# Kernel tuning notes

Measured on AMD Instinct MI355X. Metric: run time of the kernel, lower is better.

## Reference

```python
import jax, jax.numpy as jnp
import numpy as np


def setup_inputs() -> dict:
    key = jax.random.key(0)
    ks = jax.random.split(key, 6)
    B, H, W, C = 4, 64, 64, 256
    D = 256 // 4  # inter_channel // 4
    return {
        "g": jax.random.normal(ks[0], (B, H, W, C), dtype=jnp.float32),
        "x": jax.random.normal(ks[1], (B, H, W, C), dtype=jnp.float32),
        "x_query": jax.random.normal(ks[2], (B, H, W, D), dtype=jnp.float32),
        "phi_g": jax.random.normal(ks[3], (B, H, W, D), dtype=jnp.float32),
        "x_value": jax.random.normal(ks[4], (B, H, W, C), dtype=jnp.float32),
        "k": jax.random.normal(ks[5], (1,), dtype=jnp.float32),
    }


def reference(g, x, x_query, phi_g, x_value, k):
    B, H, W, C = x.shape
    D = x_query.shape[-1]
    HW = H * W
    q = x_query.reshape(B, HW, D)
    pg = phi_g.reshape(B, HW, D)
    v = x_value.reshape(B, HW, C)
    # scale[b,i,j] = sum_d phi_g[b,i,d] * x_query[b,j,d]  -> (B, HW, HW)
    scale = jnp.einsum("bid,bjd->bij", pg, q)
    soft = jax.nn.softmax(scale, axis=-1)
    # scaled_value[b,i,c] = sum_j soft[b,i,j] * v[b,j,c]
    sv = jnp.einsum("bij,bjc->bic", soft, v).reshape(B, H, W, C)
    layero = k * sv + x
    return jnp.concatenate([layero, g], axis=3)
```

## Files before the change

kernel.cpp:

```cpp
#include <hip/hip_runtime.h>

#define N_  4096
#define D_  64
#define C_  256

typedef short bf16x8 __attribute__((ext_vector_type(8)));
typedef float f32x4  __attribute__((ext_vector_type(4)));

__device__ __forceinline__ unsigned short f2bf(float f) {
    union { float f; unsigned int i; } v; v.f = f;
    unsigned int r = v.i + 0x7fffu + ((v.i >> 16) & 1u);
    return (unsigned short)(r >> 16);
}

__global__ void prepass_kernel(const float* __restrict__ xq,
                               const float* __restrict__ pg,
                               const float* __restrict__ xv,
                               unsigned short* __restrict__ qbf,
                               unsigned short* __restrict__ pgbf,
                               unsigned short* __restrict__ vt2) {
    const int bid = blockIdx.x;
    const int t   = threadIdx.x;
    if (bid < 512) {
        const float* src = (bid < 256) ? xq : pg;
        unsigned short* dst = (bid < 256) ? qbf : pgbf;
        const int base = (bid & 255) * 1024 + t;
#pragma unroll
        for (int it = 0; it < 4; ++it) {
            const int i = base + it * 256;
            float4 v = ((const float4*)src)[i];
            ushort4 o;
            o.x = f2bf(v.x); o.y = f2bf(v.y); o.z = f2bf(v.z); o.w = f2bf(v.w);
            ((ushort4*)dst)[i] = o;
        }
        return;
    }
    const int lane = t & 63;
    const int w    = t >> 6;
    const int l15  = lane & 15;
    const int quad = lane >> 4;
    const int f    = (bid - 512) * 4 + w;
    const int b    = f >> 11;
    const int jt   = (f >> 6) & 31;
    const int cb   = (f >> 2) & 15;
    const int ks   = f & 3;
    const int c    = cb * 16 + l15;
    const int jb   = jt * 128 + ks * 32 + quad * 8;
    const float* src = xv + ((size_t)b * N_ + jb) * C_ + c;
    float v0 = src[0 * C_], v1 = src[1 * C_], v2 = src[2 * C_], v3 = src[3 * C_];
    float v4 = src[4 * C_], v5 = src[5 * C_], v6 = src[6 * C_], v7 = src[7 * C_];
    uint4 o;
    o.x = (unsigned)f2bf(v0) | ((unsigned)f2bf(v1) << 16);
    o.y = (unsigned)f2bf(v2) | ((unsigned)f2bf(v3) << 16);
    o.z = (unsigned)f2bf(v4) | ((unsigned)f2bf(v5) << 16);
    o.w = (unsigned)f2bf(v6) | ((unsigned)f2bf(v7) << 16);
    *(uint4*)(vt2 + (size_t)f * 512 + lane * 8) = o;
}

__global__ __launch_bounds__(512, 2) void attn_main(
    const float* __restrict__ g,  const float* __restrict__ x,
    const float* __restrict__ kk, float* __restrict__ out,
    const unsigned short* __restrict__ qbf,
    const unsigned short* __restrict__ pgbf,
    const unsigned short* __restrict__ vt2)
{
    __shared__ __align__(16) unsigned char smem[69632];
    __shared__ float s_l[64];

    const int t    = threadIdx.x;
    const int lane = t & 63;
    const int w    = t >> 6;
    const int l15  = lane & 15;
    const int quad = lane >> 4;
    const int swz  = (l15 & 7) << 4;
    const int jh   = w >> 2;
    const int ch4  = w & 3;

    const int bid = blockIdx.x;
    const int b   = bid & 3;
    const int rg  = bid >> 2;
    const int i0  = rg * 64;
    const size_t rowbase = (size_t)b * N_ + i0;

    if (t < 64) s_l[t] = 0.f;

#pragma unroll
    for (int it = 0; it < 8; ++it) {
        const int row = it * 8 + w;
        const int c4  = lane * 4;
        const float4 gv = *(const float4*)(g + (rowbase + row) * C_ + c4);
        *(float4*)(out + (rowbase + row) * (2 * C_) + C_ + c4) = gv;
    }

    bf16x8 pgf[4][2];
#pragma unroll
    for (int nt = 0; nt < 4; ++nt)
#pragma unroll
        for (int ks = 0; ks < 2; ++ks)
            pgf[nt][ks] = *(const bf16x8*)(pgbf +
                (rowbase + nt * 16 + l15) * D_ + ks * 32 + quad * 8);

    f32x4 oacc[4][4];
#pragma unroll
    for (int mt = 0; mt < 4; ++mt)
#pragma unroll
        for (int ct = 0; ct < 4; ++ct)
            oacc[mt][ct] = (f32x4){0.f, 0.f, 0.f, 0.f};
    float ls[4] = {0.f, 0.f, 0.f, 0.f};

    const unsigned short* qb  = qbf + (size_t)b * N_ * D_;
    const unsigned short* vtb = vt2 + (size_t)b * N_ * C_;
    unsigned short* const pb0 = (unsigned short*)smem;
    unsigned short* const pb1 = (unsigned short*)(smem + 16384);

    auto load_q = [&](bf16x8 (&qf)[2], int jt) {
#pragma unroll
        for (int ks = 0; ks < 2; ++ks)
            qf[ks] = *(const bf16x8*)(qb +
                (size_t)(jt * 128 + w * 16 + l15) * D_ + ks * 32 + quad * 8);
    };
    auto load_v = [&](bf16x8 (&vf)[2][4], int jt) {
#pragma unroll
        for (int ks2 = 0; ks2 < 2; ++ks2)
#pragma unroll
            for (int ct = 0; ct < 4; ++ct)
                vf[ks2][ct] = *(const bf16x8*)(vtb +
                    ((size_t)(jt * 16 + ch4 * 4 + ct) * 4 + (jh * 2 + ks2)) * 512 +
                    (size_t)lane * 8);
    };
    auto s_step = [&](const bf16x8 (&qf)[2], unsigned short* pbuf) {
        f32x4 sacc[4];
#pragma unroll
        for (int nt = 0; nt < 4; ++nt) sacc[nt] = (f32x4){0.f,0.f,0.f,0.f};
#pragma unroll
        for (int ks = 0; ks < 2; ++ks)
#pragma unroll
            for (int nt = 0; nt < 4; ++nt)
                sacc[nt] = __builtin_amdgcn_mfma_f32_16x16x32_bf16(
                    qf[ks], pgf[nt][ks], sacc[nt], 0, 0, 0);
#pragma unroll
        for (int nt = 0; nt < 4; ++nt) {
            const float p0 = __expf(sacc[nt][0]);
            const float p1 = __expf(sacc[nt][1]);
            const float p2 = __expf(sacc[nt][2]);
            const float p3 = __expf(sacc[nt][3]);
            ls[nt] += (p0 + p1) + (p2 + p3);
            ushort4 pk;
            pk.x = f2bf(p0); pk.y = f2bf(p1); pk.z = f2bf(p2); pk.w = f2bf(p3);
            const int wb = ((nt * 16 + l15) * 256 + (w * 16 + quad * 4) * 2) ^ swz;
            *(ushort4*)((char*)pbuf + wb) = pk;
        }
    };
    auto pv_step = [&](const bf16x8 (&vf)[2][4], const unsigned short* pbuf) {
#pragma unroll
        for (int ks2 = 0; ks2 < 2; ++ks2) {
            const int ks = jh * 2 + ks2;
            bf16x8 pa[4];
#pragma unroll
            for (int mt = 0; mt < 4; ++mt) {
                const int rb = ((mt * 16 + l15) * 256 + ks * 64 + quad * 16) ^ swz;
                pa[mt] = *(const bf16x8*)((const char*)pbuf + rb);
            }
#pragma unroll
            for (int ct = 0; ct < 4; ++ct)
#pragma unroll
                for (int mt = 0; mt < 4; ++mt)
                    oacc[mt][ct] = __builtin_amdgcn_mfma_f32_16x16x32_bf16(
                        pa[mt], vf[ks2][ct], oacc[mt][ct], 0, 0, 0);
        }
    };

    bf16x8 qfA[2], qfB[2], vfA[2][4], vfB[2][4];

    load_q(qfA, 0);
    load_v(vfA, 0);
    s_step(qfA, pb0);
    load_q(qfB, 1);
    __syncthreads();

#pragma unroll 1
    for (int jtp = 0; jtp < 15; ++jtp) {
        const int p = 2 * jtp;
        load_v(vfB, p + 1);
        load_q(qfA, p + 2);
        s_step(qfB, pb1);
        pv_step(vfA, pb0);
        __syncthreads();
        load_v(vfA, p + 2);
        load_q(qfB, p + 3);
        s_step(qfA, pb0);
        pv_step(vfB, pb1);
        __syncthreads();
    }
    load_v(vfB, 31);
    s_step(qfB, pb1);
    pv_step(vfA, pb0);
    __syncthreads();
    pv_step(vfB, pb1);

#pragma unroll
    for (int nt = 0; nt < 4; ++nt) {
        float s = ls[nt];
        s += __shfl_xor(s, 16);
        s += __shfl_xor(s, 32);
        if (lane < 16) atomicAdd(&s_l[nt * 16 + lane], s);
    }
    __syncthreads();

    {
        float* Rg = (float*)(smem + (size_t)ch4 * 17408);
        if (jh == 1) {
#pragma unroll
            for (int mt = 0; mt < 4; ++mt)
#pragma unroll
                for (int ct = 0; ct < 4; ++ct)
#pragma unroll
                    for (int r = 0; r < 4; ++r)
                        Rg[(mt * 16 + quad * 4 + r) * 68 + ct * 16 + l15] = oacc[mt][ct][r];
        }
        __syncthreads();
        if (jh == 0) {
#pragma unroll
            for (int mt = 0; mt < 4; ++mt)
#pragma unroll
                for (int ct = 0; ct < 4; ++ct)
#pragma unroll
                    for (int r = 0; r < 4; ++r) {
                        const int idx = (mt * 16 + quad * 4 + r) * 68 + ct * 16 + l15;
                        Rg[idx] += oacc[mt][ct][r];
                    }
        }
        __syncthreads();
    }

    const float kval = kk[0];
#pragma unroll
    for (int it = 0; it < 8; ++it) {
        const int idx = it * 512 + t;
        const int row = idx >> 6;
        const int cq  = idx & 63;
        const int c   = cq * 4;
        const float* Rg = (const float*)(smem + (size_t)(cq >> 4) * 17408);
        const f32x4 ov = *(const f32x4*)&Rg[row * 68 + (cq & 15) * 4];
        const float linv = 1.f / s_l[row];
        const size_t rr = rowbase + row;
        const float4 xv4 = *(const float4*)(x + rr * C_ + c);
        float4 o4;
        o4.x = kval * (ov[0] * linv) + xv4.x;
        o4.y = kval * (ov[1] * linv) + xv4.y;
        o4.z = kval * (ov[2] * linv) + xv4.z;
        o4.w = kval * (ov[3] * linv) + xv4.w;
        *(float4*)(out + rr * (2 * C_) + c) = o4;
    }
}

#define ROWS 4
#define FNT  256
__global__ __launch_bounds__(FNT, 2) void attn_fallback(
    const float* __restrict__ g, const float* __restrict__ x,
    const float* __restrict__ xq, const float* __restrict__ pg,
    const float* __restrict__ xv, const float* __restrict__ kk,
    float* __restrict__ out)
{
    __shared__ __align__(16) float s_pg[ROWS][D_];
    __shared__ __align__(16) float s_sc[N_ * ROWS];
    __shared__ float s_rmax[4][ROWS];
    __shared__ float s_rsum[4][ROWS];

    const int t = threadIdx.x, lane = t & 63, w = t >> 6, blk = blockIdx.x;
    const int b = blk >> 10, i0 = (blk & 1023) * ROWS;
    const size_t rowbase = (size_t)b * N_ + i0;
    {
        const int r = t >> 6, cc = (t & 63) * 4;
        const float4 gv = *(const float4*)(g + (rowbase + r) * C_ + cc);
        *(float4*)(out + (rowbase + r) * (2 * C_) + C_ + cc) = gv;
    }
    { const int r = t >> 6, d = t & 63; s_pg[r][d] = pg[(rowbase + r) * D_ + d]; }
    __syncthreads();
    const float* qb = xq + (size_t)b * N_ * D_;
    float lmax[ROWS];
#pragma unroll
    for (int r = 0; r < ROWS; ++r) lmax[r] = -1e30f;
    for (int jj = 0; jj < N_ / FNT; ++jj) {
        const int j = t + jj * FNT;
        const float4* q4p = (const float4*)(qb + (size_t)j * D_);
        float s[ROWS] = {0.f, 0.f, 0.f, 0.f};
#pragma unroll
        for (int u = 0; u < D_ / 8; ++u) {
            const float4 qa = q4p[u * 2], qc = q4p[u * 2 + 1];
#pragma unroll
            for (int r = 0; r < ROWS; ++r) {
                const float4 pa = *(const float4*)&s_pg[r][u * 8];
                const float4 pb = *(const float4*)&s_pg[r][u * 8 + 4];
                s[r] += qa.x * pa.x + qa.y * pa.y + qa.z * pa.z + qa.w * pa.w
                      + qc.x * pb.x + qc.y * pb.y + qc.z * pb.z + qc.w * pb.w;
            }
        }
        *(float4*)&s_sc[j * ROWS] = make_float4(s[0], s[1], s[2], s[3]);
#pragma unroll
        for (int r = 0; r < ROWS; ++r) lmax[r] = fmaxf(lmax[r], s[r]);
    }
#pragma unroll
    for (int r = 0; r < ROWS; ++r) {
        float m = lmax[r];
        for (int o = 32; o > 0; o >>= 1) m = fmaxf(m, __shfl_down(m, o));
        if (lane == 0) s_rmax[w][r] = m;
    }
    __syncthreads();
    float bmax[ROWS];
#pragma unroll
    for (int r = 0; r < ROWS; ++r)
        bmax[r] = fmaxf(fmaxf(s_rmax[0][r], s_rmax[1][r]), fmaxf(s_rmax[2][r], s_rmax[3][r]));
    float lsum[ROWS] = {0.f, 0.f, 0.f, 0.f};
    for (int jj = 0; jj < N_ / FNT; ++jj) {
        const int j = t + jj * FNT;
        float4 s4 = *(const float4*)&s_sc[j * ROWS];
        s4.x = __expf(s4.x - bmax[0]); s4.y = __expf(s4.y - bmax[1]);
        s4.z = __expf(s4.z - bmax[2]); s4.w = __expf(s4.w - bmax[3]);
        *(float4*)&s_sc[j * ROWS] = s4;
        lsum[0] += s4.x; lsum[1] += s4.y; lsum[2] += s4.z; lsum[3] += s4.w;
    }
#pragma unroll
    for (int r = 0; r < ROWS; ++r) {
        float sm = lsum[r];
        for (int o = 32; o > 0; o >>= 1) sm += __shfl_down(sm, o);
        if (lane == 0) s_rsum[w][r] = sm;
    }
    __syncthreads();
    float rinv[ROWS];
#pragma unroll
    for (int r = 0; r < ROWS; ++r)
        rinv[r] = 1.f / (s_rsum[0][r] + s_rsum[1][r] + s_rsum[2][r] + s_rsum[3][r]);
    const int jg = lane >> 4;
    const int c0 = (w * 16 + (lane & 15)) * 4;
    const float* vb = xv + (size_t)b * N_ * C_;
    float acc[ROWS][4];
#pragma unroll
    for (int r = 0; r < ROWS; ++r)
#pragma unroll
        for (int q = 0; q < 4; ++q) acc[r][q] = 0.f;
#pragma unroll 4
    for (int jj = 0; jj < N_ / 4; ++jj) {
        const int j = jj * 4 + jg;
        const float4 p4 = *(const float4*)&s_sc[j * ROWS];
        const float4 v4 = *(const float4*)(vb + (size_t)j * C_ + c0);
        acc[0][0] += p4.x * v4.x; acc[0][1] += p4.x * v4.y; acc[0][2] += p4.x * v4.z; acc[0][3] += p4.x * v4.w;
        acc[1][0] += p4.y * v4.x; acc[1][1] += p4.y * v4.y; acc[1][2] += p4.y * v4.z; acc[1][3] += p4.y * v4.w;
        acc[2][0] += p4.z * v4.x; acc[2][1] += p4.z * v4.y; acc[2][2] += p4.z * v4.z; acc[2][3] += p4.z * v4.w;
        acc[3][0] += p4.w * v4.x; acc[3][1] += p4.w * v4.y; acc[3][2] += p4.w * v4.z; acc[3][3] += p4.w * v4.w;
    }
#pragma unroll
    for (int r = 0; r < ROWS; ++r)
#pragma unroll
        for (int q = 0; q < 4; ++q) {
            acc[r][q] += __shfl_xor(acc[r][q], 16);
            acc[r][q] += __shfl_xor(acc[r][q], 32);
        }
    const float kval = kk[0];
    if (lane < 16) {
        const int c = (w * 16 + lane) * 4;
#pragma unroll
        for (int r = 0; r < ROWS; ++r) {
            const float4 xv4 = *(const float4*)(x + (rowbase + r) * C_ + c);
            float4 ov;
            ov.x = kval * (acc[r][0] * rinv[r]) + xv4.x;
            ov.y = kval * (acc[r][1] * rinv[r]) + xv4.y;
            ov.z = kval * (acc[r][2] * rinv[r]) + xv4.z;
            ov.w = kval * (acc[r][3] * rinv[r]) + xv4.w;
            *(float4*)(out + (rowbase + r) * (2 * C_) + c) = ov;
        }
    }
}

extern "C" void kernel_launch(void* const* d_in, const int* in_sizes, int n_in,
                              void* d_out, int out_size, void* d_ws, size_t ws_size,
                              hipStream_t stream) {
    const float* g  = (const float*)d_in[0];
    const float* x  = (const float*)d_in[1];
    const float* xq = (const float*)d_in[2];
    const float* pg = (const float*)d_in[3];
    const float* xv = (const float*)d_in[4];
    const float* kk = (const float*)d_in[5];
    float* out = (float*)d_out;

    const int B = in_sizes[0] / (N_ * C_);
    const size_t qn = (size_t)B * N_ * D_;
    const size_t vn = (size_t)B * N_ * C_;
    const size_t need = (2 * qn + vn) * sizeof(unsigned short);

    if (B != 4 || ws_size < need) {
        attn_fallback<<<dim3(B * (N_ / ROWS)), FNT, 0, stream>>>(g, x, xq, pg, xv, kk, out);
        return;
    }

    unsigned short* qbf  = (unsigned short*)d_ws;
    unsigned short* pgbf = qbf + qn;
    unsigned short* vt2  = pgbf + qn;

    prepass_kernel<<<dim3(512 + B * 512), 256, 0, stream>>>(xq, pg, xv, qbf, pgbf, vt2);
    attn_main<<<dim3(B * (N_ / 64)), 512, 0, stream>>>(g, x, kk, out, qbf, pgbf, vt2);
}
```

Before: 160.4 us.

## Split attention blocks across channel halves with 256-thread blocks

Each 512-thread block that handled 64 query rows across all 256 channels becomes two 256-thread blocks, each owning 128 output channels. The grid doubles, and each wave now computes two score strips. The point is finer-grained scheduling and lower per-block register and LDS use. The cost is that every channel half recomputes the QK^T scores and exponentials, and the V register double-buffering is dropped, so V loads happen in the same phase as their use. s_setprio is also raised around the PV MFMA bursts.

Result: slower. 176.3 us (+9.9%).

```diff
diff --git a/kernel.cpp b/kernel.cpp
--- a/kernel.cpp
+++ b/kernel.cpp
@@ -57,14 +57,14 @@
     *(uint4*)(vt2 + (size_t)f * 512 + lane * 8) = o;
 }
 
-__global__ __launch_bounds__(512, 2) void attn_main(
+__global__ __launch_bounds__(256, 2) void attn_main(
     const float* __restrict__ g,  const float* __restrict__ x,
     const float* __restrict__ kk, float* __restrict__ out,
     const unsigned short* __restrict__ qbf,
     const unsigned short* __restrict__ pgbf,
     const unsigned short* __restrict__ vt2)
 {
-    __shared__ __align__(16) unsigned char smem[69632];
+    __shared__ __align__(16) unsigned char smem[34816];
     __shared__ float s_l[64];
 
     const int t    = threadIdx.x;
@@ -73,23 +73,27 @@
     const int l15  = lane & 15;
     const int quad = lane >> 4;
     const int swz  = (l15 & 7) << 4;
-    const int jh   = w >> 2;
-    const int ch4  = w & 3;
-
-    const int bid = blockIdx.x;
-    const int b   = bid & 3;
-    const int rg  = bid >> 2;
-    const int i0  = rg * 64;
+    const int jh   = w >> 1;
+    const int ch2  = w & 1;
+
+    const int bid  = blockIdx.x;
+    const int b    = bid & 3;
+    const int cblk = (bid >> 2) & 1;
+    const int rg   = bid >> 3;
+    const int i0   = rg * 64;
+    const int c0   = cblk * 128;
     const size_t rowbase = (size_t)b * N_ + i0;
 
     if (t < 64) s_l[t] = 0.f;
 
 #pragma unroll
     for (int it = 0; it < 8; ++it) {
-        const int row = it * 8 + w;
-        const int c4  = lane * 4;
-        const float4 gv = *(const float4*)(g + (rowbase + row) * C_ + c4);
-        *(float4*)(out + (rowbase + row) * (2 * C_) + C_ + c4) = gv;
+        const int idx = it * 256 + t;
+        const int row = idx >> 5;
+        const int cq  = idx & 31;
+        const int c   = c0 + cq * 4;
+        const float4 gv = *(const float4*)(g + (rowbase + row) * C_ + c);
+        *(float4*)(out + (rowbase + row) * (2 * C_) + C_ + c) = gv;
     }
 
     bf16x8 pgf[4][2];
@@ -113,11 +117,15 @@
     unsigned short* const pb0 = (unsigned short*)smem;
     unsigned short* const pb1 = (unsigned short*)(smem + 16384);
 
-    auto load_q = [&](bf16x8 (&qf)[2], int jt) {
-#pragma unroll
-        for (int ks = 0; ks < 2; ++ks)
-            qf[ks] = *(const bf16x8*)(qb +
-                (size_t)(jt * 128 + w * 16 + l15) * D_ + ks * 32 + quad * 8);
+    auto load_q = [&](bf16x8 (&qf)[2][2], int jt) {
+        const int jtc = (jt < 31) ? jt : 31;
+#pragma unroll
+        for (int s = 0; s < 2; ++s)
+#pragma unroll
+            for (int ks = 0; ks < 2; ++ks)
+                qf[s][ks] = *(const bf16x8*)(qb +
+                    (size_t)(jtc * 128 + (w + s * 4) * 16 + l15) * D_ +
+                    ks * 32 + quad * 8);
     };
     auto load_v = [&](bf16x8 (&vf)[2][4], int jt) {
 #pragma unroll
@@ -125,30 +133,35 @@
 #pragma unroll
             for (int ct = 0; ct < 4; ++ct)
                 vf[ks2][ct] = *(const bf16x8*)(vtb +
-                    ((size_t)(jt * 16 + ch4 * 4 + ct) * 4 + (jh * 2 + ks2)) * 512 +
-                    (size_t)lane * 8);
+                    ((size_t)(jt * 16 + cblk * 8 + ch2 * 4 + ct) * 4 +
+                     (jh * 2 + ks2)) * 512 + (size_t)lane * 8);
     };
-    auto s_step = [&](const bf16x8 (&qf)[2], unsigned short* pbuf) {
-        f32x4 sacc[4];
-#pragma unroll
-        for (int nt = 0; nt < 4; ++nt) sacc[nt] = (f32x4){0.f,0.f,0.f,0.f};
-#pragma unroll
-        for (int ks = 0; ks < 2; ++ks)
-#pragma unroll
-            for (int nt = 0; nt < 4; ++nt)
-                sacc[nt] = __builtin_amdgcn_mfma_f32_16x16x32_bf16(
-                    qf[ks], pgf[nt][ks], sacc[nt], 0, 0, 0);
-#pragma unroll
-        for (int nt = 0; nt < 4; ++nt) {
-            const float p0 = __expf(sacc[nt][0]);
-            const float p1 = __expf(sacc[nt][1]);
-            const float p2 = __expf(sacc[nt][2]);
-            const float p3 = __expf(sacc[nt][3]);
-            ls[nt] += (p0 + p1) + (p2 + p3);
-            ushort4 pk;
-            pk.x = f2bf(p0); pk.y = f2bf(p1); pk.z = f2bf(p2); pk.w = f2bf(p3);
-            const int wb = ((nt * 16 + l15) * 256 + (w * 16 + quad * 4) * 2) ^ swz;
-            *(ushort4*)((char*)pbuf + wb) = pk;
+    auto s_step = [&](const bf16x8 (&qf)[2][2], unsigned short* pbuf) {
+#pragma unroll
+        for (int s = 0; s < 2; ++s) {
+            const int strip = w + s * 4;
+            f32x4 sacc[4];
+#pragma unroll
+            for (int nt = 0; nt < 4; ++nt) sacc[nt] = (f32x4){0.f,0.f,0.f,0.f};
+#pragma unroll
+            for (int ks = 0; ks < 2; ++ks)
+#pragma unroll
+                for (int nt = 0; nt < 4; ++nt)
+                    sacc[nt] = __builtin_amdgcn_mfma_f32_16x16x32_bf16(
+                        qf[s][ks], pgf[nt][ks], sacc[nt], 0, 0, 0);
+#pragma unroll
+            for (int nt = 0; nt < 4; ++nt) {
+                const float p0 = __expf(sacc[nt][0]);
+                const float p1 = __expf(sacc[nt][1]);
+                const float p2 = __expf(sacc[nt][2]);
+                const float p3 = __expf(sacc[nt][3]);
+                ls[nt] += (p0 + p1) + (p2 + p3);
+                ushort4 pk;
+                pk.x = f2bf(p0); pk.y = f2bf(p1); pk.z = f2bf(p2); pk.w = f2bf(p3);
+                const int wb = ((nt * 16 + l15) * 256 +
+                                (strip * 16 + quad * 4) * 2) ^ swz;
+                *(ushort4*)((char*)pbuf + wb) = pk;
+            }
         }
     };
     auto pv_step = [&](const bf16x8 (&vf)[2][4], const unsigned short* pbuf) {
@@ -158,22 +171,23 @@
             bf16x8 pa[4];
 #pragma unroll
             for (int mt = 0; mt < 4; ++mt) {
-                const int rb = ((mt * 16 + l15) * 256 + ks * 64 + quad * 16) ^ swz;
+                const int rb = ((mt * 16 + l15) * 256 + (ks * 32 + quad * 8) * 2) ^ swz;
                 pa[mt] = *(const bf16x8*)((const char*)pbuf + rb);
             }
+            __builtin_amdgcn_s_setprio(1);
 #pragma unroll
             for (int ct = 0; ct < 4; ++ct)
 #pragma unroll
                 for (int mt = 0; mt < 4; ++mt)
                     oacc[mt][ct] = __builtin_amdgcn_mfma_f32_16x16x32_bf16(
                         pa[mt], vf[ks2][ct], oacc[mt][ct], 0, 0, 0);
+            __builtin_amdgcn_s_setprio(0);
         }
     };
 
-    bf16x8 qfA[2], qfB[2], vfA[2][4], vfB[2][4];
+    bf16x8 qfA[2][2], qfB[2][2], vf[2][4];
 
     load_q(qfA, 0);
-    load_v(vfA, 0);
     s_step(qfA, pb0);
     load_q(qfB, 1);
     __syncthreads();
@@ -181,22 +195,23 @@
 #pragma unroll 1
     for (int jtp = 0; jtp < 15; ++jtp) {
         const int p = 2 * jtp;
-        load_v(vfB, p + 1);
+        load_v(vf, p);
         load_q(qfA, p + 2);
         s_step(qfB, pb1);
-        pv_step(vfA, pb0);
+        pv_step(vf, pb0);
         __syncthreads();
-        load_v(vfA, p + 2);
+        load_v(vf, p + 1);
         load_q(qfB, p + 3);
         s_step(qfA, pb0);
-        pv_step(vfB, pb1);
+        pv_step(vf, pb1);
         __syncthreads();
     }
-    load_v(vfB, 31);
+    load_v(vf, 30);
     s_step(qfB, pb1);
-    pv_step(vfA, pb0);
-    __syncthreads();
-    pv_step(vfB, pb1);
+    pv_step(vf, pb0);
+    __syncthreads();
+    load_v(vf, 31);
+    pv_step(vf, pb1);
 
 #pragma unroll
     for (int nt = 0; nt < 4; ++nt) {
@@ -208,7 +223,7 @@
     __syncthreads();
 
     {
-        float* Rg = (float*)(smem + (size_t)ch4 * 17408);
+        float* Rg = (float*)(smem + (size_t)ch2 * 17408);
         if (jh == 1) {
 #pragma unroll
             for (int mt = 0; mt < 4; ++mt)
@@ -216,7 +231,8 @@
                 for (int ct = 0; ct < 4; ++ct)
 #pragma unroll
                     for (int r = 0; r < 4; ++r)
-                        Rg[(mt * 16 + quad * 4 + r) * 68 + ct * 16 + l15] = oacc[mt][ct][r];
+                        Rg[(mt * 16 + quad * 4 + r) * 68 + ct * 16 + l15] =
+                            oacc[mt][ct][r];
         }
         __syncthreads();
         if (jh == 0) {
@@ -236,14 +252,14 @@
     const float kval = kk[0];
 #pragma unroll
     for (int it = 0; it < 8; ++it) {
-        const int idx = it * 512 + t;
-        const int row = idx >> 6;
-        const int cq  = idx & 63;
-        const int c   = cq * 4;
+        const int idx = it * 256 + t;
+        const int row = idx >> 5;
+        const int cq  = idx & 31;
         const float* Rg = (const float*)(smem + (size_t)(cq >> 4) * 17408);
         const f32x4 ov = *(const f32x4*)&Rg[row * 68 + (cq & 15) * 4];
         const float linv = 1.f / s_l[row];
         const size_t rr = rowbase + row;
+        const int c = c0 + cq * 4;
         const float4 xv4 = *(const float4*)(x + rr * C_ + c);
         float4 o4;
         o4.x = kval * (ov[0] * linv) + xv4.x;
@@ -398,5 +414,5 @@
     unsigned short* vt2  = pgbf + qn;
 
     prepass_kernel<<<dim3(512 + B * 512), 256, 0, stream>>>(xq, pg, xv, qbf, pgbf, vt2);
-    attn_main<<<dim3(B * (N_ / 64)), 512, 0, stream>>>(g, x, kk, out, qbf, pgbf, vt2);
+    attn_main<<<dim3(B * (N_ / 64) * 2), 256, 0, stream>>>(g, x, kk, out, qbf, pgbf, vt2);
 }
```
